# Kernel tuning notes

Hardware: AMD Instinct MI355X
Metric: run time of the kernel (lower is better)

Reference implementation:

```python
import jax, jax.numpy as jnp
import numpy as np

EMBED = 1024
ADIM = 1024
H = 16
HD = ADIM // H          # 64
RAY = 48                # ray_subdim
R = RAY // 3            # 16
SCALE = 1.0 / np.sqrt(HD)
NB = 768                # boundary tokens
MN = 8                  # max neighbors
FG = 6                  # face_group
L = 1024                # tokens per face
B = 12                  # b * face_group
STAGES = 4


def _apply_dray(x, d, einsum_str, inverse):
    ray = x[..., :RAY].reshape(x.shape[:-1] + (3, R))
    if inverse:
        d = jnp.swapaxes(d, -1, -2)
    ray = jnp.einsum(einsum_str, d, ray).reshape(x.shape[:-1] + (RAY,))
    return jnp.concatenate([ray, x[..., RAY:]], axis=-1)


def setup_inputs() -> dict:
    key = jax.random.key(0)
    ks = jax.random.split(key, 12)
    inp = {}
    inp['x'] = jax.random.normal(ks[0], (B, L, EMBED), dtype=jnp.float32)
    inp['qkv_w'] = jax.random.normal(ks[1], (EMBED, 3 * ADIM), dtype=jnp.float32) * 0.02
    inp['out_w'] = jax.random.normal(ks[2], (ADIM, EMBED), dtype=jnp.float32) * 0.02
    inp['out_b'] = jax.random.normal(ks[3], (EMBED,), dtype=jnp.float32) * 0.02
    inp['d_ray'] = jax.random.normal(ks[4], (STAGES, FG, L, 3, 3), dtype=jnp.float32)
    inp['boundary_face_ids'] = jax.random.randint(ks[5], (NB,), 0, FG, dtype=jnp.int32).astype(jnp.int64)
    inp['boundary_token_indices'] = jnp.arange(NB, dtype=jnp.int64)
    inp['boundary_local_indices'] = jax.random.randint(ks[6], (NB,), 0, L, dtype=jnp.int32).astype(jnp.int64)
    inp['boundary_stage_ids'] = jax.random.randint(ks[7], (NB,), 0, STAGES, dtype=jnp.int32).astype(jnp.int64)
    inp['neighbor_face_ids'] = jax.random.randint(ks[8], (NB, MN), 0, FG, dtype=jnp.int32).astype(jnp.int64)
    inp['neighbor_token_indices'] = jax.random.randint(ks[9], (NB, MN), 0, L, dtype=jnp.int32).astype(jnp.int64)
    inp['neighbor_local_indices'] = jax.random.randint(ks[10], (NB, MN), 0, L, dtype=jnp.int32).astype(jnp.int64)
    inp['neighbor_stage_ids'] = jax.random.randint(ks[11], (NB, MN), 0, STAGES, dtype=jnp.int32).astype(jnp.int64)
    inp['neighbor_mask'] = jnp.ones((NB, MN), dtype=bool)
    inp['face_group'] = FG
    return inp


def reference(x, qkv_w, out_w, out_b, d_ray,
              boundary_face_ids, boundary_token_indices, boundary_local_indices, boundary_stage_ids,
              neighbor_face_ids, neighbor_token_indices, neighbor_local_indices, neighbor_stage_ids,
              neighbor_mask, face_group):
    b = x.shape[0] // face_group
    l = x.shape[1]
    xt = x.reshape(b, face_group, l, EMBED)          # [b, FG, L, E]
    max_face, max_idx = face_group - 1, l - 1

    qf = jnp.clip(boundary_face_ids, 0, max_face)
    qi = jnp.clip(boundary_token_indices, 0, max_idx)
    valid_q = (boundary_face_ids == qf) & (boundary_token_indices == qi)

    nf = jnp.clip(neighbor_face_ids, 0, max_face)
    ni = jnp.clip(neighbor_token_indices, 0, max_idx)
    mask = neighbor_mask & (neighbor_face_ids == nf) & (neighbor_token_indices == ni)

    # gather boundary queries and neighbor keys/values
    x_q = xt[:, qf, qi, :]                            # [b, NB, E]
    x_kv = xt[:, nf, ni, :]                           # [b, NB, MN, E]
    q = (x_q @ qkv_w)[..., :ADIM]
    kv = x_kv @ qkv_w
    k = kv[..., ADIM:2 * ADIM]
    v = kv[..., 2 * ADIM:]

    nb, mn = q.shape[1], k.shape[2]
    q = q.reshape(b, nb, H, HD)
    k = k.reshape(b, nb, mn, H, HD)
    v = v.reshape(b, nb, mn, H, HD)

    d_q = d_ray[boundary_stage_ids, boundary_face_ids, boundary_local_indices]     # [NB, 3, 3]
    d_k = d_ray[neighbor_stage_ids,
                jnp.maximum(neighbor_face_ids, 0),
                jnp.maximum(neighbor_local_indices, 0)]                            # [NB, MN, 3, 3]

    q = _apply_dray(q, d_q, 'nij,bnhjr->bnhir', inverse=False)
    k = _apply_dray(k, d_k, 'nmij,bnmhjr->bnmhir', inverse=False)
    v = _apply_dray(v, d_k, 'nmij,bnmhjr->bnmhir', inverse=False)

    attn = jnp.einsum('bnhd,bnmhd->bnmh', q, k) * SCALE
    attn = jnp.where(mask[None, :, :, None], attn, -jnp.inf)
    attn = jax.nn.softmax(attn, axis=2)               # softmax over neighbors
    out = jnp.einsum('bnmh,bnmhd->bnhd', attn, v)

    out = _apply_dray(out, d_q, 'nij,bnhjr->bnhir', inverse=True)
    out = out.reshape(b, nb, ADIM) @ out_w + out_b
    out = out * valid_q[None, :, None].astype(out.dtype)

    out_full = jnp.zeros_like(xt).at[:, qf, qi, :].set(out)
    return out_full.reshape(-1, l, EMBED)
```

## Files before the change

kernel.cpp:

```cpp
#include <hip/hip_runtime.h>
#include <hip/hip_bf16.h>
#include <cstddef>

#define FG 6
#define L 1024
#define NB 768
#define MN 8
#define H 16
#define HD 64
#define ADIM 1024
#define STAGES 4
#define SCALE 0.125f

typedef __attribute__((ext_vector_type(8))) short bf16x8;
typedef __attribute__((ext_vector_type(4))) float f32x4;
typedef __attribute__((address_space(3))) short lds_short_t;
typedef const __attribute__((address_space(1))) short g_short_t;

__device__ __forceinline__ int clampi(int v, int lo, int hi) {
  return v < lo ? lo : (v > hi ? hi : v);
}

__device__ __forceinline__ short f2bf(float f) {
  __hip_bfloat16 h = __float2bfloat16(f);
  return *reinterpret_cast<short*>(&h);
}

__device__ __forceinline__ void gload16(const short* g, short* l) {
  __builtin_amdgcn_global_load_lds((g_short_t*)g, (lds_short_t*)l, 16, 0, 0);
}

__global__ __launch_bounds__(256)
void conv_bf16(const float* __restrict__ in, short* __restrict__ out) {
  size_t i = ((size_t)blockIdx.x * 256 + threadIdx.x) * 8;
  float4 a = *(const float4*)(in + i);
  float4 b = *(const float4*)(in + i + 4);
  bf16x8 v;
  v[0] = f2bf(a.x); v[1] = f2bf(a.y); v[2] = f2bf(a.z); v[3] = f2bf(a.w);
  v[4] = f2bf(b.x); v[5] = f2bf(b.y); v[6] = f2bf(b.z); v[7] = f2bf(b.w);
  *(bf16x8*)(out + i) = v;
}

__global__ __launch_bounds__(256)
void transpose_both(const float* __restrict__ qkv_w, short* __restrict__ qwT,
                    const float* __restrict__ out_w, short* __restrict__ owT) {
  const int z = blockIdx.z;
  if (z == 1 && blockIdx.x >= 32) return;
  const float* in = z ? out_w : qkv_w;
  short* out = z ? owT : qwT;
  const int N = z ? 1024 : 3072;
  __shared__ float tile[32][33];
  const int n0 = blockIdx.x * 32, k0 = blockIdx.y * 32;
  const int tx = threadIdx.x & 31, ty = threadIdx.x >> 5;
  #pragma unroll
  for (int i = 0; i < 4; ++i)
    tile[ty + i * 8][tx] = in[(size_t)(k0 + ty + i * 8) * N + n0 + tx];
  __syncthreads();
  #pragma unroll
  for (int i = 0; i < 4; ++i)
    out[(size_t)(n0 + ty + i * 8) * 1024 + k0 + tx] =
        f2bf(tile[tx][ty + i * 8]);
}

__global__ __launch_bounds__(256)
void q_gemm64(const short* __restrict__ A, const short* __restrict__ B,
              float* __restrict__ C,
              const int* __restrict__ f_ids, const int* __restrict__ t_ids)
{
  __shared__ __align__(16) short As[4096];
  __shared__ __align__(16) short Bs[8192];

  const int tid = threadIdx.x;
  const int w = tid >> 6, lane = tid & 63;
  const int row0 = blockIdx.y * 64, col0 = blockIdx.x * 128;
  const int lr = lane & 15, lq = lane >> 4;
  const int wrow = (w >> 1) * 32, wcol = (w & 1) * 64;

  size_t asrc[2]; short* adst[2];
  #pragma unroll
  for (int c = 0; c < 2; ++c) {
    const int d = c * 256 + tid, r = d >> 3;
    const int ss = (d & 7) ^ (r & 7);
    const int rr = row0 + r;
    const int bi = rr >= NB;
    const int idx = rr - bi * NB;
    const int f = clampi(f_ids[idx], 0, FG - 1);
    const int q = clampi(t_ids[idx], 0, L - 1);
    asrc[c] = (size_t)((bi * FG + f) * L + q) * 1024 + ss * 8;
    adst[c] = As + d * 8;
  }
  size_t bsrc[4]; short* bdst[4];
  #pragma unroll
  for (int c = 0; c < 4; ++c) {
    const int d = c * 256 + tid, r = d >> 3;
    const int ss = (d & 7) ^ (r & 7);
    bsrc[c] = (size_t)(col0 + r) * 1024 + ss * 8;
    bdst[c] = Bs + d * 8;
  }

  const char* As8 = (const char*)As;
  const char* Bs8 = (const char*)Bs;
  const int swz = lr & 7;

  f32x4 acc[2][4];
  #pragma unroll
  for (int m = 0; m < 2; ++m)
    #pragma unroll
    for (int n = 0; n < 4; ++n) acc[m][n] = (f32x4){0.f, 0.f, 0.f, 0.f};

  for (int kt = 0; kt < 16; ++kt) {
    #pragma unroll
    for (int c = 0; c < 2; ++c) gload16(A + asrc[c] + kt * 64, adst[c]);
    #pragma unroll
    for (int c = 0; c < 4; ++c) gload16(B + bsrc[c] + kt * 64, bdst[c]);
    __syncthreads();
    #pragma unroll
    for (int kk = 0; kk < 2; ++kk) {
      const int so = ((kk * 4 + lq) ^ swz) << 4;
      bf16x8 av[2], bv[4];
      #pragma unroll
      for (int m = 0; m < 2; ++m)
        av[m] = *(const bf16x8*)(As8 + (wrow + m * 16 + lr) * 128 + so);
      #pragma unroll
      for (int n = 0; n < 4; ++n)
        bv[n] = *(const bf16x8*)(Bs8 + (wcol + n * 16 + lr) * 128 + so);
      #pragma unroll
      for (int m = 0; m < 2; ++m)
        #pragma unroll
        for (int n = 0; n < 4; ++n)
          acc[m][n] = __builtin_amdgcn_mfma_f32_16x16x32_bf16(
              av[m], bv[n], acc[m][n], 0, 0, 0);
    }
    __syncthreads();
  }

  #pragma unroll
  for (int m = 0; m < 2; ++m)
    #pragma unroll
    for (int j = 0; j < 4; ++j) {
      const int r = row0 + wrow + m * 16 + lq * 4 + j;
      #pragma unroll
      for (int n = 0; n < 4; ++n)
        C[(size_t)r * 1024 + col0 + wcol + n * 16 + lr] = acc[m][n][j];
    }
}


#define BAR()   do { __builtin_amdgcn_s_barrier(); __builtin_amdgcn_sched_barrier(0); } while (0)
#define LGKM(N) do { asm volatile("s_waitcnt lgkmcnt(" #N ")" ::: "memory"); __builtin_amdgcn_sched_barrier(0); } while (0)
#define VMC(N)  do { asm volatile("s_waitcnt vmcnt(" #N ")" ::: "memory"); __builtin_amdgcn_sched_barrier(0); } while (0)
#define PRIO1   __builtin_amdgcn_s_setprio(1)
#define PRIO0   __builtin_amdgcn_s_setprio(0)

#define LDA6(D, FB, KK, BUF)                                                  \
  { _Pragma("unroll")                                                         \
    for (int f_ = 0; f_ < 3; ++f_) {                                          \
      const int row_ = (2 * ((FB) + f_) + wm) * 16 + lr;                      \
      D[f_] = *(const bf16x8*)(As8 + (BUF) * 24576 + row_ * 128               \
               + ((((KK) * 4 + lq) ^ swz) << 4));                             \
    } }

#define LDB4(D, KK, BUF)                                                      \
  { _Pragma("unroll")                                                         \
    for (int g_ = 0; g_ < 4; ++g_) {                                          \
      const int row_ = wn * 64 + g_ * 16 + lr;                                \
      D[g_] = *(const bf16x8*)(Bs8 + (BUF) * 32768 + row_ * 128               \
               + ((((KK) * 4 + lq) ^ swz) << 4));                             \
    } }

#define MM6(AV, BV, FB)                                                       \
  { _Pragma("unroll")                                                         \
    for (int f_ = 0; f_ < 3; ++f_)                                            \
      _Pragma("unroll")                                                       \
      for (int g_ = 0; g_ < 4; ++g_)                                          \
        acc[(FB) + f_][g_] = __builtin_amdgcn_mfma_f32_16x16x32_bf16(         \
            AV[f_], BV[g_], acc[(FB) + f_][g_], 0, 0, 0); }

__global__ __launch_bounds__(512, 2)
void kv_gemm192(const short* __restrict__ A, const short* __restrict__ B,
                short* __restrict__ C,
                const int* __restrict__ f_ids, const int* __restrict__ t_ids)
{
  __shared__ __align__(16) short As[24576];
  __shared__ __align__(16) short Bs[32768];

  const int tid = threadIdx.x;
  const int w = tid >> 6, lane = tid & 63;
  const int wm = w >> 2, wn = w & 3;
  const int lr = lane & 15, lq = lane >> 4;
  const int row0 = blockIdx.y * 192;
  const int col0 = blockIdx.x * 256;

  const int ssrc = (((tid & 7) ^ ((tid >> 3) & 7))) * 8;

  size_t a_src[3];
  #pragma unroll
  for (int c = 0; c < 3; ++c) {
    const int rr = row0 + c * 64 + (tid >> 3);
    const int bi = rr >= NB * MN;
    const int idx = rr - bi * (NB * MN);
    const int f = clampi(f_ids[idx], 0, FG - 1);
    const int q = clampi(t_ids[idx], 0, L - 1);
    a_src[c] = (size_t)((bi * FG + f) * L + q) * 1024 + ssrc;
  }
  size_t b_src[2][2];
  #pragma unroll
  for (int h = 0; h < 2; ++h)
    #pragma unroll
    for (int i = 0; i < 2; ++i)
      b_src[h][i] = (size_t)(1024 + col0 + h * 128 + ((tid + i * 512) >> 3)) * 1024 + ssrc;

  auto stgA = [&](int c, int kt, int buf) {
    gload16(A + a_src[c] + kt * 64, As + buf * 12288 + c * 4096 + tid * 8);
  };
  auto stgB = [&](int h, int kt, int buf) {
    gload16(B + b_src[h][0] + kt * 64, Bs + buf * 16384 + h * 8192 + tid * 8);
    gload16(B + b_src[h][1] + kt * 64, Bs + buf * 16384 + h * 8192 + 4096 + tid * 8);
  };

  const char* As8 = (const char*)As;
  const char* Bs8 = (const char*)Bs;
  const int swz = lane & 7;

  f32x4 acc[6][4];
  #pragma unroll
  for (int f = 0; f < 6; ++f)
    #pragma unroll
    for (int g = 0; g < 4; ++g) acc[f][g] = (f32x4){0.f, 0.f, 0.f, 0.f};

  bf16x8 avA[3], avB[3], bv0[4], bv1[4];

  stgB(0, 0, 0); stgB(1, 0, 0); stgA(0, 0, 0); stgA(1, 0, 0); stgA(2, 0, 0);
  stgB(0, 1, 1); stgB(1, 1, 1); stgA(0, 1, 1);
  VMC(5); BAR();

  for (int I = 0; I < 7; ++I) {
    const int kA = 2 * I + 1, kB = 2 * I + 2, kC = 2 * I + 3;
    LDA6(avA, 0, 0, 0); LDB4(bv0, 0, 0); stgA(1, kA, 1);
    BAR(); LGKM(0); PRIO1; MM6(avA, bv0, 0); PRIO0; BAR();
    LDA6(avB, 0, 1, 0); LDB4(bv1, 1, 0); stgA(2, kA, 1);
    BAR(); LGKM(0); PRIO1; MM6(avB, bv1, 0); PRIO0; BAR();
    LDA6(avA, 3, 0, 0); stgB(0, kB, 0);
    BAR(); LGKM(0); PRIO1; MM6(avA, bv0, 3); PRIO0; BAR();
    LDA6(avB, 3, 1, 0); stgB(1, kB, 0); stgA(0, kB, 0);
    BAR(); LGKM(0); PRIO1; MM6(avB, bv1, 3); PRIO0; VMC(5); BAR();
    LDA6(avA, 0, 0, 1); LDB4(bv0, 0, 1); stgA(1, kB, 0);
    BAR(); LGKM(0); PRIO1; MM6(avA, bv0, 0); PRIO0; BAR();
    LDA6(avB, 0, 1, 1); LDB4(bv1, 1, 1); stgA(2, kB, 0);
    BAR(); LGKM(0); PRIO1; MM6(avB, bv1, 0); PRIO0; BAR();
    LDA6(avA, 3, 0, 1); stgB(0, kC, 1);
    BAR(); LGKM(0); PRIO1; MM6(avA, bv0, 3); PRIO0; BAR();
    LDA6(avB, 3, 1, 1); stgB(1, kC, 1); stgA(0, kC, 1);
    BAR(); LGKM(0); PRIO1; MM6(avB, bv1, 3); PRIO0; VMC(5); BAR();
  }

  {
    LDA6(avA, 0, 0, 0); LDB4(bv0, 0, 0); stgA(1, 15, 1);
    BAR(); LGKM(0); PRIO1; MM6(avA, bv0, 0); PRIO0; BAR();

    LDA6(avB, 0, 1, 0); LDB4(bv1, 1, 0); stgA(2, 15, 1);
    BAR(); LGKM(0); PRIO1; MM6(avB, bv1, 0); PRIO0; BAR();

    LDA6(avA, 3, 0, 0);
    BAR(); LGKM(0); PRIO1; MM6(avA, bv0, 3); PRIO0; BAR();

    LDA6(avB, 3, 1, 0);
    BAR(); LGKM(0); PRIO1; MM6(avB, bv1, 3); PRIO0; VMC(0); BAR();

    LDA6(avA, 0, 0, 1); LDB4(bv0, 0, 1);
    BAR(); LGKM(0); PRIO1; MM6(avA, bv0, 0); PRIO0; BAR();

    LDA6(avB, 0, 1, 1); LDB4(bv1, 1, 1);
    BAR(); LGKM(0); PRIO1; MM6(avB, bv1, 0); PRIO0; BAR();

    LDA6(avA, 3, 0, 1);
    BAR(); LGKM(0); PRIO1; MM6(avA, bv0, 3); PRIO0; BAR();

    LDA6(avB, 3, 1, 1);
    BAR(); LGKM(0); PRIO1; MM6(avB, bv1, 3); PRIO0;
  }

  #pragma unroll
  for (int f = 0; f < 6; ++f) {
    #pragma unroll
    for (int j = 0; j < 4; ++j) {
      const int r = row0 + (2 * f + wm) * 16 + lq * 4 + j;
      short* cp = C + (size_t)r * 2048 + col0 + wn * 64 + lr;
      #pragma unroll
      for (int g = 0; g < 4; ++g)
        cp[g * 16] = f2bf(acc[f][g][j]);
    }
  }
}

__global__ __launch_bounds__(256)
void out_gemm64(const short* __restrict__ A, const short* __restrict__ B,
                float* __restrict__ C,
                const int* __restrict__ f_ids, const int* __restrict__ t_ids,
                const float* __restrict__ bias)
{
  __shared__ __align__(16) short As[4096];
  __shared__ __align__(16) short Bs[8192];

  const int tid = threadIdx.x;
  const int w = tid >> 6, lane = tid & 63;
  const int row0 = blockIdx.y * 64, col0 = blockIdx.x * 128;
  const int lr = lane & 15, lq = lane >> 4;
  const int wrow = (w >> 1) * 32, wcol = (w & 1) * 64;

  size_t asrc[2]; short* adst[2];
  #pragma unroll
  for (int c = 0; c < 2; ++c) {
    const int d = c * 256 + tid, r = d >> 3;
    const int ss = (d & 7) ^ (r & 7);
    asrc[c] = (size_t)(row0 + r) * 1024 + ss * 8;
    adst[c] = As + d * 8;
  }
  size_t bsrc[4]; short* bdst[4];
  #pragma unroll
  for (int c = 0; c < 4; ++c) {
    const int d = c * 256 + tid, r = d >> 3;
    const int ss = (d & 7) ^ (r & 7);
    bsrc[c] = (size_t)(col0 + r) * 1024 + ss * 8;
    bdst[c] = Bs + d * 8;
  }

  const char* As8 = (const char*)As;
  const char* Bs8 = (const char*)Bs;
  const int swz = lr & 7;

  f32x4 acc[2][4];
  #pragma unroll
  for (int m = 0; m < 2; ++m)
    #pragma unroll
    for (int n = 0; n < 4; ++n) acc[m][n] = (f32x4){0.f, 0.f, 0.f, 0.f};

  for (int kt = 0; kt < 16; ++kt) {
    #pragma unroll
    for (int c = 0; c < 2; ++c) gload16(A + asrc[c] + kt * 64, adst[c]);
    #pragma unroll
    for (int c = 0; c < 4; ++c) gload16(B + bsrc[c] + kt * 64, bdst[c]);
    __syncthreads();
    #pragma unroll
    for (int kk = 0; kk < 2; ++kk) {
      const int so = ((kk * 4 + lq) ^ swz) << 4;
      bf16x8 av[2], bv[4];
      #pragma unroll
      for (int m = 0; m < 2; ++m)
        av[m] = *(const bf16x8*)(As8 + (wrow + m * 16 + lr) * 128 + so);
      #pragma unroll
      for (int n = 0; n < 4; ++n)
        bv[n] = *(const bf16x8*)(Bs8 + (wcol + n * 16 + lr) * 128 + so);
      #pragma unroll
      for (int m = 0; m < 2; ++m)
        #pragma unroll
        for (int n = 0; n < 4; ++n)
          acc[m][n] = __builtin_amdgcn_mfma_f32_16x16x32_bf16(
              av[m], bv[n], acc[m][n], 0, 0, 0);
    }
    __syncthreads();
  }

  float bb[4];
  #pragma unroll
  for (int n = 0; n < 4; ++n) bb[n] = bias[col0 + wcol + n * 16 + lr];
  #pragma unroll
  for (int m = 0; m < 2; ++m)
    #pragma unroll
    for (int j = 0; j < 4; ++j) {
      const int r  = row0 + wrow + m * 16 + lq * 4 + j;
      const int bi = r >= NB;
      const int nn = r - bi * NB;
      const int bf = f_ids[nn], bt = t_ids[nn];
      const int qf = clampi(bf, 0, FG - 1), qi = clampi(bt, 0, L - 1);
      const bool valid = (bf == qf) && (bt == qi);
      const size_t obase = ((size_t)(bi * FG + qf) * L + qi) * 1024;
      #pragma unroll
      for (int n = 0; n < 4; ++n) {
        const int col = col0 + wcol + n * 16 + lr;
        C[obase + col] = valid ? (acc[m][n][j] + bb[n]) : 0.f;
      }
    }
}

__global__ __launch_bounds__(256)
void attn_kernel(const float* __restrict__ dray,
                 const int* __restrict__ bfid, const int* __restrict__ blid,
                 const int* __restrict__ bsid,
                 const int* __restrict__ nfid, const int* __restrict__ ntid,
                 const int* __restrict__ nlid, const int* __restrict__ nsid,
                 const int* __restrict__ nmask,
                 const float* __restrict__ qbuf,
                 const __hip_bfloat16* __restrict__ kvbuf,
                 __hip_bfloat16* __restrict__ obuf)
{
  const int lane = threadIdx.x & 63;
  const int gw   = blockIdx.x * 4 + (threadIdx.x >> 6);
  const int h    = gw & (H - 1);
  const int bn   = gw >> 4;
  const int n    = bn % NB;

  int st = clampi(bsid[n], 0, STAGES - 1);
  int f  = clampi(bfid[n], 0, FG - 1);
  int lc = clampi(blid[n], 0, L - 1);
  const float* dqp = dray + ((size_t)(st * FG + f) * L + lc) * 9;
  float dq[9];
  #pragma unroll
  for (int t = 0; t < 9; ++t) dq[t] = dqp[t];

  const float qraw = qbuf[(size_t)bn * ADIM + h * HD + lane];
  const int rr = lane & 15;

  float x0 = __shfl(qraw, rr), x1 = __shfl(qraw, 16 + rr), x2 = __shfl(qraw, 32 + rr);
  float q0 = dq[0]*x0 + dq[1]*x1 + dq[2]*x2;
  float q1 = dq[3]*x0 + dq[4]*x1 + dq[5]*x2;
  float q2 = dq[6]*x0 + dq[7]*x1 + dq[8]*x2;
  float qd = lane < 16 ? q0 : lane < 32 ? q1 : lane < 48 ? q2 : qraw;

  const __hip_bfloat16* kvb = kvbuf + (size_t)bn * MN * 2048 + h * HD;
  float s[MN], vd[MN];
  #pragma unroll
  for (int m = 0; m < MN; ++m) {
    const int idx = n * MN + m;
    int nst = clampi(nsid[idx], 0, STAGES - 1);
    int nfc = clampi(nfid[idx], 0, FG - 1);
    int nlc = clampi(nlid[idx], 0, L - 1);
    const float* dkp = dray + ((size_t)(nst * FG + nfc) * L + nlc) * 9;
    float dk[9];
    #pragma unroll
    for (int t = 0; t < 9; ++t) dk[t] = dkp[t];

    float kraw = __bfloat162float(kvb[(size_t)m * 2048 + lane]);
    float k0 = __shfl(kraw, rr), k1 = __shfl(kraw, 16 + rr), k2 = __shfl(kraw, 32 + rr);
    float kr0 = dk[0]*k0 + dk[1]*k1 + dk[2]*k2;
    float kr1 = dk[3]*k0 + dk[4]*k1 + dk[5]*k2;
    float kr2 = dk[6]*k0 + dk[7]*k1 + dk[8]*k2;
    float kd = lane < 16 ? kr0 : lane < 32 ? kr1 : lane < 48 ? kr2 : kraw;

    float p = qd * kd;
    #pragma unroll
    for (int off = 32; off; off >>= 1) p += __shfl_xor(p, off);
    s[m] = p;

    float vraw = __bfloat162float(kvb[(size_t)m * 2048 + 1024 + lane]);
    float v0 = __shfl(vraw, rr), v1 = __shfl(vraw, 16 + rr), v2 = __shfl(vraw, 32 + rr);
    float vr0 = dk[0]*v0 + dk[1]*v1 + dk[2]*v2;
    float vr1 = dk[3]*v0 + dk[4]*v1 + dk[5]*v2;
    float vr2 = dk[6]*v0 + dk[7]*v1 + dk[8]*v2;
    vd[m] = lane < 16 ? vr0 : lane < 32 ? vr1 : lane < 48 ? vr2 : vraw;
  }

  float mx = -INFINITY;
  #pragma unroll
  for (int m = 0; m < MN; ++m) {
    const int idx = n * MN + m;
    int nf = nfid[idx], nt = ntid[idx];
    bool ok = (nmask[idx] != 0) && nf >= 0 && nf < FG && nt >= 0 && nt < L;
    s[m] = ok ? s[m] * SCALE : -INFINITY;
    mx = fmaxf(mx, s[m]);
  }
  float den = 0.f;
  #pragma unroll
  for (int m = 0; m < MN; ++m) { s[m] = expf(s[m] - mx); den += s[m]; }
  float inv = 1.0f / den;

  float od = 0.f;
  #pragma unroll
  for (int m = 0; m < MN; ++m) od += s[m] * vd[m];
  od *= inv;

  float y0 = __shfl(od, rr), y1 = __shfl(od, 16 + rr), y2 = __shfl(od, 32 + rr);
  float t0 = dq[0]*y0 + dq[3]*y1 + dq[6]*y2;
  float t1 = dq[1]*y0 + dq[4]*y1 + dq[7]*y2;
  float t2 = dq[2]*y0 + dq[5]*y1 + dq[8]*y2;
  float outd = lane < 16 ? t0 : lane < 32 ? t1 : lane < 48 ? t2 : od;

  obuf[(size_t)bn * ADIM + h * HD + lane] = __float2bfloat16(outd);
}

extern "C" void kernel_launch(void* const* d_in, const int* in_sizes, int n_in,
                              void* d_out, int out_size, void* d_ws, size_t ws_size,
                              hipStream_t stream) {
  const float* x     = (const float*)d_in[0];
  const float* qkv_w = (const float*)d_in[1];
  const float* out_w = (const float*)d_in[2];
  const float* out_b = (const float*)d_in[3];
  const float* dray  = (const float*)d_in[4];
  const int* bfid  = (const int*)d_in[5];
  const int* btid  = (const int*)d_in[6];
  const int* blid  = (const int*)d_in[7];
  const int* bsid  = (const int*)d_in[8];
  const int* nfid  = (const int*)d_in[9];
  const int* ntid  = (const int*)d_in[10];
  const int* nlid  = (const int*)d_in[11];
  const int* nsid  = (const int*)d_in[12];
  const int* nmask = (const int*)d_in[13];

  char* ws = (char*)d_ws;
  short* xb    = (short*)(ws);
  short* qwT   = (short*)(ws + 25165824);
  short* owT   = (short*)(ws + 31457280);
  float* qbuf  = (float*)(ws + 33554432);
  short* kvbuf = (short*)(ws + 39845888);
  short* obuf  = (short*)(ws + 90177536);

  (void)hipMemsetAsync(d_out, 0, (size_t)out_size * sizeof(float), stream);

  conv_bf16<<<6144, 256, 0, stream>>>(x, xb);
  transpose_both<<<dim3(96, 32, 2), 256, 0, stream>>>(qkv_w, qwT, out_w, owT);

  q_gemm64<<<dim3(8, 24), 256, 0, stream>>>(xb, qwT, qbuf, bfid, btid);
  kv_gemm192<<<dim3(8, 64), 512, 0, stream>>>(xb, qwT, kvbuf, nfid, ntid);
  attn_kernel<<<6144, 256, 0, stream>>>(dray, bfid, blid, bsid,
                                        nfid, ntid, nlid, nsid, nmask,
                                        qbuf, (const __hip_bfloat16*)kvbuf,
                                        (__hip_bfloat16*)obuf);
  out_gemm64<<<dim3(8, 24), 256, 0, stream>>>(obuf, owT, (float*)d_out,
                                              bfid, btid, out_b);
}
```

Before: 165.7 us.

## Fuse output zeroing into prep kernel and restructure attention per boundary token

Replaces the separate memset of the output with a zero-fill folded into the bf16 conversion kernel, which is launched with twice as many blocks so it covers the whole output. The attention kernel now uses one block per (batch, boundary token). Each block stages that token's K/V rows into LDS with direct global-to-LDS loads and computes the rotation matrices and mask once in shared memory, then loops over 4 heads per wave. This removes the redundant per-head reloads of index data and rotation matrices, at the cost of 32KB of LDS per block, which limits occupancy.

```diff
diff --git a/kernel.cpp b/kernel.cpp
--- a/kernel.cpp
+++ b/kernel.cpp
@@ -26,12 +26,21 @@
   return *reinterpret_cast<short*>(&h);
 }
 
+__device__ __forceinline__ float bf2f(short s) {
+  __hip_bfloat16 h = *reinterpret_cast<__hip_bfloat16*>(&s);
+  return __bfloat162float(h);
+}
+
 __device__ __forceinline__ void gload16(const short* g, short* l) {
   __builtin_amdgcn_global_load_lds((g_short_t*)g, (lds_short_t*)l, 16, 0, 0);
 }
 
 __global__ __launch_bounds__(256)
-void conv_bf16(const float* __restrict__ in, short* __restrict__ out) {
+void prep_kernel(const float* __restrict__ in, short* __restrict__ out,
+                 float* __restrict__ zout) {
+  const size_t zi = ((size_t)blockIdx.x * 256 + threadIdx.x) * 4;
+  *(float4*)(zout + zi) = (float4){0.f, 0.f, 0.f, 0.f};
+  if (blockIdx.x >= 6144) return;
   size_t i = ((size_t)blockIdx.x * 256 + threadIdx.x) * 8;
   float4 a = *(const float4*)(in + i);
   float4 b = *(const float4*)(in + i + 4);
@@ -144,7 +153,6 @@
         C[(size_t)r * 1024 + col0 + wcol + n * 16 + lr] = acc[m][n][j];
     }
 }
-
 
 #define BAR()   do { __builtin_amdgcn_s_barrier(); __builtin_amdgcn_sched_barrier(0); } while (0)
 #define LGKM(N) do { asm volatile("s_waitcnt lgkmcnt(" #N ")" ::: "memory"); __builtin_amdgcn_sched_barrier(0); } while (0)
@@ -384,98 +392,118 @@
 }
 
 __global__ __launch_bounds__(256)
-void attn_kernel(const float* __restrict__ dray,
-                 const int* __restrict__ bfid, const int* __restrict__ blid,
-                 const int* __restrict__ bsid,
-                 const int* __restrict__ nfid, const int* __restrict__ ntid,
-                 const int* __restrict__ nlid, const int* __restrict__ nsid,
-                 const int* __restrict__ nmask,
-                 const float* __restrict__ qbuf,
-                 const __hip_bfloat16* __restrict__ kvbuf,
-                 __hip_bfloat16* __restrict__ obuf)
+void attn_kernel2(const float* __restrict__ dray,
+                  const int* __restrict__ bfid, const int* __restrict__ blid,
+                  const int* __restrict__ bsid,
+                  const int* __restrict__ nfid, const int* __restrict__ ntid,
+                  const int* __restrict__ nlid, const int* __restrict__ nsid,
+                  const int* __restrict__ nmask,
+                  const float* __restrict__ qbuf,
+                  const short* __restrict__ kvbuf,
+                  __hip_bfloat16* __restrict__ obuf)
 {
-  const int lane = threadIdx.x & 63;
-  const int gw   = blockIdx.x * 4 + (threadIdx.x >> 6);
-  const int h    = gw & (H - 1);
-  const int bn   = gw >> 4;
+  __shared__ __align__(16) short kvlds[MN * 2048];
+  __shared__ float smdq[9];
+  __shared__ float smdk[MN][9];
+  __shared__ int   smok[MN];
+
+  const int bn   = blockIdx.x;
   const int n    = bn % NB;
-
-  int st = clampi(bsid[n], 0, STAGES - 1);
-  int f  = clampi(bfid[n], 0, FG - 1);
-  int lc = clampi(blid[n], 0, L - 1);
-  const float* dqp = dray + ((size_t)(st * FG + f) * L + lc) * 9;
-  float dq[9];
-  #pragma unroll
-  for (int t = 0; t < 9; ++t) dq[t] = dqp[t];
-
-  const float qraw = qbuf[(size_t)bn * ADIM + h * HD + lane];
-  const int rr = lane & 15;
-
-  float x0 = __shfl(qraw, rr), x1 = __shfl(qraw, 16 + rr), x2 = __shfl(qraw, 32 + rr);
-  float q0 = dq[0]*x0 + dq[1]*x1 + dq[2]*x2;
-  float q1 = dq[3]*x0 + dq[4]*x1 + dq[5]*x2;
-  float q2 = dq[6]*x0 + dq[7]*x1 + dq[8]*x2;
-  float qd = lane < 16 ? q0 : lane < 32 ? q1 : lane < 48 ? q2 : qraw;
-
-  const __hip_bfloat16* kvb = kvbuf + (size_t)bn * MN * 2048 + h * HD;
-  float s[MN], vd[MN];
-  #pragma unroll
-  for (int m = 0; m < MN; ++m) {
+  const int tid  = threadIdx.x;
+  const int w    = tid >> 6, lane = tid & 63;
+
+  const short* kvb = kvbuf + (size_t)bn * MN * 2048;
+  #pragma unroll
+  for (int j = 0; j < 8; ++j)
+    gload16(kvb + (j * 256 + tid) * 8, kvlds + (j * 256 + tid) * 8);
+
+  if (tid < 9) {
+    int st = clampi(bsid[n], 0, STAGES - 1);
+    int f  = clampi(bfid[n], 0, FG - 1);
+    int lc = clampi(blid[n], 0, L - 1);
+    smdq[tid] = dray[((size_t)(st * FG + f) * L + lc) * 9 + tid];
+  } else if (tid >= 64 && tid < 136) {
+    const int t = tid - 64, m = t / 9, j = t - m * 9;
     const int idx = n * MN + m;
     int nst = clampi(nsid[idx], 0, STAGES - 1);
     int nfc = clampi(nfid[idx], 0, FG - 1);
     int nlc = clampi(nlid[idx], 0, L - 1);
-    const float* dkp = dray + ((size_t)(nst * FG + nfc) * L + nlc) * 9;
-    float dk[9];
-    #pragma unroll
-    for (int t = 0; t < 9; ++t) dk[t] = dkp[t];
-
-    float kraw = __bfloat162float(kvb[(size_t)m * 2048 + lane]);
-    float k0 = __shfl(kraw, rr), k1 = __shfl(kraw, 16 + rr), k2 = __shfl(kraw, 32 + rr);
-    float kr0 = dk[0]*k0 + dk[1]*k1 + dk[2]*k2;
-    float kr1 = dk[3]*k0 + dk[4]*k1 + dk[5]*k2;
-    float kr2 = dk[6]*k0 + dk[7]*k1 + dk[8]*k2;
-    float kd = lane < 16 ? kr0 : lane < 32 ? kr1 : lane < 48 ? kr2 : kraw;
-
-    float p = qd * kd;
-    #pragma unroll
-    for (int off = 32; off; off >>= 1) p += __shfl_xor(p, off);
-    s[m] = p;
-
-    float vraw = __bfloat162float(kvb[(size_t)m * 2048 + 1024 + lane]);
-    float v0 = __shfl(vraw, rr), v1 = __shfl(vraw, 16 + rr), v2 = __shfl(vraw, 32 + rr);
-    float vr0 = dk[0]*v0 + dk[1]*v1 + dk[2]*v2;
-    float vr1 = dk[3]*v0 + dk[4]*v1 + dk[5]*v2;
-    float vr2 = dk[6]*v0 + dk[7]*v1 + dk[8]*v2;
-    vd[m] = lane < 16 ? vr0 : lane < 32 ? vr1 : lane < 48 ? vr2 : vraw;
-  }
-
-  float mx = -INFINITY;
-  #pragma unroll
-  for (int m = 0; m < MN; ++m) {
+    smdk[m][j] = dray[((size_t)(nst * FG + nfc) * L + nlc) * 9 + j];
+  } else if (tid >= 192 && tid < 192 + MN) {
+    const int m = tid - 192;
     const int idx = n * MN + m;
     int nf = nfid[idx], nt = ntid[idx];
-    bool ok = (nmask[idx] != 0) && nf >= 0 && nf < FG && nt >= 0 && nt < L;
-    s[m] = ok ? s[m] * SCALE : -INFINITY;
-    mx = fmaxf(mx, s[m]);
-  }
-  float den = 0.f;
-  #pragma unroll
-  for (int m = 0; m < MN; ++m) { s[m] = expf(s[m] - mx); den += s[m]; }
-  float inv = 1.0f / den;
-
-  float od = 0.f;
-  #pragma unroll
-  for (int m = 0; m < MN; ++m) od += s[m] * vd[m];
-  od *= inv;
-
-  float y0 = __shfl(od, rr), y1 = __shfl(od, 16 + rr), y2 = __shfl(od, 32 + rr);
-  float t0 = dq[0]*y0 + dq[3]*y1 + dq[6]*y2;
-  float t1 = dq[1]*y0 + dq[4]*y1 + dq[7]*y2;
-  float t2 = dq[2]*y0 + dq[5]*y1 + dq[8]*y2;
-  float outd = lane < 16 ? t0 : lane < 32 ? t1 : lane < 48 ? t2 : od;
-
-  obuf[(size_t)bn * ADIM + h * HD + lane] = __float2bfloat16(outd);
+    smok[m] = (nmask[idx] != 0) && nf >= 0 && nf < FG && nt >= 0 && nt < L;
+  }
+  __syncthreads();
+
+  float dq[9];
+  #pragma unroll
+  for (int t = 0; t < 9; ++t) dq[t] = smdq[t];
+
+  const int rr = lane & 15;
+
+  for (int hi = 0; hi < 4; ++hi) {
+    const int h = hi * 4 + w;
+
+    const float qraw = qbuf[(size_t)bn * ADIM + h * HD + lane];
+    float x0 = __shfl(qraw, rr), x1 = __shfl(qraw, 16 + rr), x2 = __shfl(qraw, 32 + rr);
+    float q0 = dq[0]*x0 + dq[1]*x1 + dq[2]*x2;
+    float q1 = dq[3]*x0 + dq[4]*x1 + dq[5]*x2;
+    float q2 = dq[6]*x0 + dq[7]*x1 + dq[8]*x2;
+    float qd = lane < 16 ? q0 : lane < 32 ? q1 : lane < 48 ? q2 : qraw;
+
+    float s[MN], vd[MN];
+    #pragma unroll
+    for (int m = 0; m < MN; ++m) {
+      float dk[9];
+      #pragma unroll
+      for (int t = 0; t < 9; ++t) dk[t] = smdk[m][t];
+
+      float kraw = bf2f(kvlds[m * 2048 + h * HD + lane]);
+      float k0 = __shfl(kraw, rr), k1 = __shfl(kraw, 16 + rr), k2 = __shfl(kraw, 32 + rr);
+      float kr0 = dk[0]*k0 + dk[1]*k1 + dk[2]*k2;
+      float kr1 = dk[3]*k0 + dk[4]*k1 + dk[5]*k2;
+      float kr2 = dk[6]*k0 + dk[7]*k1 + dk[8]*k2;
+      float kd = lane < 16 ? kr0 : lane < 32 ? kr1 : lane < 48 ? kr2 : kraw;
+
+      float p = qd * kd;
+      #pragma unroll
+      for (int off = 32; off; off >>= 1) p += __shfl_xor(p, off);
+      s[m] = p;
+
+      float vraw = bf2f(kvlds[m * 2048 + 1024 + h * HD + lane]);
+      float v0 = __shfl(vraw, rr), v1 = __shfl(vraw, 16 + rr), v2 = __shfl(vraw, 32 + rr);
+      float vr0 = dk[0]*v0 + dk[1]*v1 + dk[2]*v2;
+      float vr1 = dk[3]*v0 + dk[4]*v1 + dk[5]*v2;
+      float vr2 = dk[6]*v0 + dk[7]*v1 + dk[8]*v2;
+      vd[m] = lane < 16 ? vr0 : lane < 32 ? vr1 : lane < 48 ? vr2 : vraw;
+    }
+
+    float mx = -INFINITY;
+    #pragma unroll
+    for (int m = 0; m < MN; ++m) {
+      s[m] = smok[m] ? s[m] * SCALE : -INFINITY;
+      mx = fmaxf(mx, s[m]);
+    }
+    float den = 0.f;
+    #pragma unroll
+    for (int m = 0; m < MN; ++m) { s[m] = expf(s[m] - mx); den += s[m]; }
+    float inv = 1.0f / den;
+
+    float od = 0.f;
+    #pragma unroll
+    for (int m = 0; m < MN; ++m) od += s[m] * vd[m];
+    od *= inv;
+
+    float y0 = __shfl(od, rr), y1 = __shfl(od, 16 + rr), y2 = __shfl(od, 32 + rr);
+    float t0 = dq[0]*y0 + dq[3]*y1 + dq[6]*y2;
+    float t1 = dq[1]*y0 + dq[4]*y1 + dq[7]*y2;
+    float t2 = dq[2]*y0 + dq[5]*y1 + dq[8]*y2;
+    float outd = lane < 16 ? t0 : lane < 32 ? t1 : lane < 48 ? t2 : od;
+
+    obuf[(size_t)bn * ADIM + h * HD + lane] = __float2bfloat16(outd);
+  }
 }
 
 extern "C" void kernel_launch(void* const* d_in, const int* in_sizes, int n_in,
@@ -504,17 +532,15 @@
   short* kvbuf = (short*)(ws + 39845888);
   short* obuf  = (short*)(ws + 90177536);
 
-  (void)hipMemsetAsync(d_out, 0, (size_t)out_size * sizeof(float), stream);
-
-  conv_bf16<<<6144, 256, 0, stream>>>(x, xb);
+  prep_kernel<<<12288, 256, 0, stream>>>(x, xb, (float*)d_out);
   transpose_both<<<dim3(96, 32, 2), 256, 0, stream>>>(qkv_w, qwT, out_w, owT);
 
   q_gemm64<<<dim3(8, 24), 256, 0, stream>>>(xb, qwT, qbuf, bfid, btid);
   kv_gemm192<<<dim3(8, 64), 512, 0, stream>>>(xb, qwT, kvbuf, nfid, ntid);
-  attn_kernel<<<6144, 256, 0, stream>>>(dray, bfid, blid, bsid,
-                                        nfid, ntid, nlid, nsid, nmask,
-                                        qbuf, (const __hip_bfloat16*)kvbuf,
-                                        (__hip_bfloat16*)obuf);
+  attn_kernel2<<<1536, 256, 0, stream>>>(dray, bfid, blid, bsid,
+                                         nfid, ntid, nlid, nsid, nmask,
+                                         qbuf, kvbuf,
+                                         (__hip_bfloat16*)obuf);
   out_gemm64<<<dim3(8, 24), 256, 0, stream>>>(obuf, owT, (float*)d_out,
                                               bfid, btid, out_b);
 }
```

After: 158.7 us. 1.04x faster.
